# Optimization experiments

Hardware: AMD Instinct MI355X
Metric: run time of the kernel (lower is better)

## Reference

```python
import jax, jax.numpy as jnp
import numpy as np

DIM, HEADS, HDIM, B, L = 2048, 16, 128, 2, 2048

def setup_inputs() -> dict:
    key = jax.random.key(0)
    ks = jax.random.split(key, 7)
    s = 1.0 / np.sqrt(DIM)
    return {
        "x": jax.random.normal(ks[0], (B, L, DIM), jnp.float32),
        "rope_emb": jax.random.uniform(ks[1], (L, HDIM), jnp.float32),
        "wq": jax.random.normal(ks[2], (DIM, DIM), jnp.float32) * s,
        "wk": jax.random.normal(ks[3], (DIM, DIM), jnp.float32) * s,
        "wv": jax.random.normal(ks[4], (DIM, DIM), jnp.float32) * s,
        "wo": jax.random.normal(ks[5], (DIM, DIM), jnp.float32) * s,
        "bo": jnp.zeros((DIM,), jnp.float32),
    }

def _rotate_half(x):
    x1, x2 = jnp.split(x, 2, axis=-1)
    return jnp.concatenate((-x2, x1), axis=-1)

def reference(x, rope_emb, wq, wk, wv, wo, bo):
    Bq, Lq, D = x.shape
    # projections; torch Linear: y = x @ W.T, weights here stored as [out,in]
    q = jnp.einsum("bld,ed->ble", x, wq).reshape(Bq, Lq, HEADS, HDIM).transpose(0, 2, 1, 3)
    k = jnp.einsum("bld,ed->ble", x, wk).reshape(Bq, Lq, HEADS, HDIM).transpose(0, 2, 1, 3)
    v = jnp.einsum("bld,ed->ble", x, wv).reshape(Bq, Lq, HEADS, HDIM).transpose(0, 2, 1, 3)
    cos = jnp.cos(rope_emb)[None, None]  # [1,1,L,hd]
    sin = jnp.sin(rope_emb)[None, None]
    q = q * cos + _rotate_half(q) * sin
    k = k * cos + _rotate_half(k) * sin
    scale = HDIM ** -0.5
    attn = jnp.einsum("bhqd,bhkd->bhqk", q, k) * scale
    attn = jax.nn.softmax(attn, axis=-1)
    out = jnp.einsum("bhqk,bhkd->bhqd", attn, v)
    out = out.transpose(0, 2, 1, 3).reshape(Bq, Lq, D)
    return jnp.einsum("bld,ed->ble", out, wo) + bo
```

## Files before the change

kernel.cpp:

```cpp
#include <hip/hip_runtime.h>
#include <hip/hip_bf16.h>
#include <stdint.h>

#define DIMS  2048
#define HEADS 16
#define HD    128
#define BATCH 2
#define SEQ   2048
#define MROWS (BATCH*SEQ)
#define QKVN  (3*DIMS)

using bf16x8 = __attribute__((ext_vector_type(8))) short;
using f32x4  = __attribute__((ext_vector_type(4))) float;
using f32x16 = __attribute__((ext_vector_type(16))) float;
using u16x4  = __attribute__((ext_vector_type(4))) unsigned short;

__device__ __forceinline__ unsigned short f2b(float f){
    __hip_bfloat16 h = __float2bfloat16(f);
    return *reinterpret_cast<unsigned short*>(&h);
}
__device__ __forceinline__ float b2f(unsigned short u){
    __hip_bfloat16 h;
    *reinterpret_cast<unsigned short*>(&h) = u;
    return __bfloat162float(h);
}
__device__ __forceinline__ unsigned int pkbf(float lo, float hi){
    return (unsigned int)f2b(lo) | ((unsigned int)f2b(hi) << 16);
}

__device__ __forceinline__ void glds16(const void* g, void* l){
    __builtin_amdgcn_global_load_lds(
        (const __attribute__((address_space(1))) unsigned int*)g,
        (__attribute__((address_space(3))) unsigned int*)l, 16, 0, 0);
}


__global__ void k_f32bf16(const float* __restrict__ src, unsigned short* __restrict__ dst, int n4){
    int i = blockIdx.x*blockDim.x + threadIdx.x;
    if (i >= n4) return;
    const float4 v = reinterpret_cast<const float4*>(src)[i];
    u16x4 o = { f2b(v.x), f2b(v.y), f2b(v.z), f2b(v.w) };
    *reinterpret_cast<u16x4*>(dst + 4*(size_t)i) = o;
}

__global__ void k_cossin(const float* __restrict__ r, float* __restrict__ c, float* __restrict__ s, int n){
    int i = blockIdx.x*blockDim.x + threadIdx.x;
    if (i >= n) return;
    float v = r[i];
    c[i] = cosf(v);
    s[i] = sinf(v);
}

__global__ void k_rope(unsigned short* __restrict__ qkv,
                       const float* __restrict__ ct, const float* __restrict__ st){
    const int idx = blockIdx.x*blockDim.x + threadIdx.x;
    const int d0 = (idx & 7) << 3;
    const int h  = (idx >> 3) & (HEADS-1);
    const int l  = (idx >> 7) & (SEQ-1);
    const int b  = idx >> 18;

    const float4* cp = reinterpret_cast<const float4*>(ct + l*HD + d0);
    const float4* sp = reinterpret_cast<const float4*>(st + l*HD + d0);
    const float4 cl0 = cp[0],  cl1 = cp[1];
    const float4 sl0 = sp[0],  sl1 = sp[1];
    const float4 cu0 = cp[16], cu1 = cp[17];
    const float4 su0 = sp[16], su1 = sp[17];
    const float cl[8] = {cl0.x,cl0.y,cl0.z,cl0.w, cl1.x,cl1.y,cl1.z,cl1.w};
    const float sl[8] = {sl0.x,sl0.y,sl0.z,sl0.w, sl1.x,sl1.y,sl1.z,sl1.w};
    const float cu[8] = {cu0.x,cu0.y,cu0.z,cu0.w, cu1.x,cu1.y,cu1.z,cu1.w};
    const float su[8] = {su0.x,su0.y,su0.z,su0.w, su1.x,su1.y,su1.z,su1.w};

    unsigned short* base = qkv + (size_t)(b*SEQ + l)*QKVN + h*HD + d0;
    #pragma unroll
    for (int s = 0; s < 2; ++s){
        unsigned short* rp = base + s*DIMS;
        bf16x8 lo = *reinterpret_cast<const bf16x8*>(rp);
        bf16x8 hi = *reinterpret_cast<const bf16x8*>(rp + 64);
        bf16x8 olo, ohi;
        #pragma unroll
        for (int j = 0; j < 8; ++j){
            const float x1 = b2f((unsigned short)lo[j]);
            const float x2 = b2f((unsigned short)hi[j]);
            olo[j] = (short)f2b(x1*cl[j] - x2*sl[j]);
            ohi[j] = (short)f2b(x2*cu[j] + x1*su[j]);
        }
        *reinterpret_cast<bf16x8*>(rp)      = olo;
        *reinterpret_cast<bf16x8*>(rp + 64) = ohi;
    }
}

__global__ void k_vtrans(const unsigned short* __restrict__ qkv, unsigned short* __restrict__ vt){
    __shared__ unsigned short t[64*68];
    const int lt = blockIdx.x;
    const int dt = blockIdx.y;
    const int bh = blockIdx.z;
    const int b = bh >> 4, h = bh & 15;
    const int tid = threadIdx.x;
    const int l0 = lt << 6;
    #pragma unroll
    for (int it = 0; it < 4; ++it){
        const int c = tid + (it<<8);
        const int l = c >> 4;
        const int d4 = (c & 15) << 2;
        const u16x4 v = *reinterpret_cast<const u16x4*>(
            qkv + (size_t)(b*SEQ + l0 + l)*QKVN + 2*DIMS + h*HD + (dt<<6) + d4);
        *reinterpret_cast<u16x4*>(&t[l*68 + d4]) = v;
    }
    __syncthreads();
    #pragma unroll
    for (int it = 0; it < 4; ++it){
        const int c = tid + (it<<8);
        const int d = c >> 4;
        const int l4 = (c & 15) << 2;
        u16x4 o = { t[(l4+0)*68 + d], t[(l4+1)*68 + d], t[(l4+2)*68 + d], t[(l4+3)*68 + d] };
        *reinterpret_cast<u16x4*>(&vt[((size_t)bh*HD + (dt<<6) + d)*SEQ + l0 + l4]) = o;
    }
}


template<int FINAL>
__global__ __launch_bounds__(256) void k_gemm_bt(
    const unsigned short* __restrict__ A, const unsigned short* __restrict__ B,
    void* __restrict__ C, const float* __restrict__ bias, int M, int N, int K)
{
    __shared__ unsigned short lA[128*64];
    __shared__ unsigned short lB[128*64];
    const int tid  = threadIdx.x;
    const int lane = tid & 63;
    const int wave = tid >> 6;

    const int nbx = N >> 7;
    const int nwg = gridDim.x;
    const int cpx = nwg >> 3;
    const int bid = blockIdx.x;
    const int wg  = (bid & 7)*cpx + (bid >> 3);
    const int m0 = (wg / nbx) << 7;
    const int n0 = (wg % nbx) << 7;

    const int wr = (wave >> 1) << 6;
    const int wc = (wave & 1) << 6;

    f32x4 acc[4][4] = {};

    const int srow_base = (wave<<3) + (lane>>3);
    const int schunk = lane & 7;

    for (int k0 = 0; k0 < K; k0 += 64){
        #pragma unroll
        for (int i = 0; i < 4; ++i){
            const int row  = (i<<5) + srow_base;
            const int scol = k0 + ((schunk ^ (row & 7)) << 3);
            glds16(A + (size_t)(m0 + row)*K + scol, &lA[((i<<5) + (wave<<3)) << 6]);
            glds16(B + (size_t)(n0 + row)*K + scol, &lB[((i<<5) + (wave<<3)) << 6]);
        }
        __syncthreads();
        #pragma unroll
        for (int ks = 0; ks < 2; ++ks){
            bf16x8 af[4], bfr[4];
            const int colbase = (ks<<5) + ((lane>>4)<<3);
            #pragma unroll
            for (int mi = 0; mi < 4; ++mi){
                const int row = wr + (mi<<4) + (lane & 15);
                af[mi] = *reinterpret_cast<const bf16x8*>(&lA[(row<<6) + (colbase ^ ((row&7)<<3))]);
            }
            #pragma unroll
            for (int ni = 0; ni < 4; ++ni){
                const int row = wc + (ni<<4) + (lane & 15);
                bfr[ni] = *reinterpret_cast<const bf16x8*>(&lB[(row<<6) + (colbase ^ ((row&7)<<3))]);
            }
            #pragma unroll
            for (int mi = 0; mi < 4; ++mi)
                #pragma unroll
                for (int ni = 0; ni < 4; ++ni)
                    acc[mi][ni] = __builtin_amdgcn_mfma_f32_16x16x32_bf16(af[mi], bfr[ni], acc[mi][ni], 0, 0, 0);
        }
        __syncthreads();
    }

    const int r0 = (lane >> 4) << 2;
    const int cn = lane & 15;
    #pragma unroll
    for (int mi = 0; mi < 4; ++mi)
        #pragma unroll
        for (int r = 0; r < 4; ++r){
            const int gm = m0 + wr + (mi<<4) + r0 + r;
            #pragma unroll
            for (int ni = 0; ni < 4; ++ni){
                const int gn = n0 + wc + (ni<<4) + cn;
                const float v = acc[mi][ni][r];
                if (FINAL)
                    reinterpret_cast<float*>(C)[(size_t)gm*N + gn] = v + bias[gn];
                else
                    reinterpret_cast<unsigned short*>(C)[(size_t)gm*N + gn] = f2b(v);
            }
        }
}


union U8 { unsigned int w[4]; bf16x8 v; };

__global__ __launch_bounds__(512, 2) void k_attn(
    const unsigned short* __restrict__ qkv, const unsigned short* __restrict__ vt,
    unsigned short* __restrict__ aout)
{
    __shared__ unsigned short lK[2][64*128];
    __shared__ unsigned short lV[2][128*64];
    __shared__ unsigned short lO[8*32*132];

    const int tid  = threadIdx.x;
    const int lane = tid & 63;
    const int wave = tid >> 6;
    const int lq   = lane & 31;
    const int hi   = lane >> 5;
    const int bh = blockIdx.y;
    const int b = bh >> 4, h = bh & 15;
    const int q0w = (blockIdx.x << 8) + (wave << 5);

    const unsigned short* Kb = qkv + (size_t)b*SEQ*QKVN + DIMS + h*HD;
    const unsigned short* Vb = vt + (size_t)bh*HD*SEQ;

    bf16x8 qf[8];
    {
        const float qscale = 0.08838834764831845f * 1.4426950408889634f;
        const unsigned short* qp = qkv + (size_t)(b*SEQ + q0w + lq)*QKVN + h*HD + (hi<<3);
        #pragma unroll
        for (int ks = 0; ks < 8; ++ks){
            bf16x8 tv = *reinterpret_cast<const bf16x8*>(qp + (ks<<4));
            #pragma unroll
            for (int j = 0; j < 8; ++j)
                tv[j] = (short)f2b(b2f((unsigned short)tv[j]) * qscale);
            qf[ks] = tv;
        }
    }

    float m_run = -3e38f, l_run = 0.f;
    f32x16 oacc[4] = {};

    #define STAGE(pb, kv0) do { \
        _Pragma("unroll") \
        for (int i = 0; i < 2; ++i){ \
            const int kr = (wave<<3) + (i<<2) + (lane>>4); \
            glds16(Kb + (size_t)((kv0) + kr)*QKVN + (((lane&15) ^ (kr&7))<<3), \
                   &lK[pb][((wave<<3) + (i<<2))<<7]); \
            const int dr = (wave<<4) + (i<<3) + (lane>>3); \
            glds16(Vb + (size_t)dr*SEQ + (kv0) + (((lane&7) ^ (dr&7))<<3), \
                   &lV[pb][((wave<<4) + (i<<3))<<6]); \
        } \
    } while(0)

    int buf = 0;
    STAGE(0, 0);
    __syncthreads();

    for (int t = 0; t < SEQ/64; ++t){
        if (t < SEQ/64 - 1) STAGE(buf^1, (t+1)*64);

        const unsigned short* Kbuf = &lK[buf][0];
        const unsigned short* Vbuf = &lV[buf][0];

        f32x16 st0 = {}, st1 = {};
        __builtin_amdgcn_s_setprio(1);
        #pragma unroll
        for (int ks = 0; ks < 8; ++ks){
            const int col = (((ks<<1) + hi) ^ (lq & 7)) << 3;
            bf16x8 k0 = *reinterpret_cast<const bf16x8*>(&Kbuf[(lq<<7) + col]);
            bf16x8 k1 = *reinterpret_cast<const bf16x8*>(&Kbuf[((32+lq)<<7) + col]);
            st0 = __builtin_amdgcn_mfma_f32_32x32x16_bf16(k0, qf[ks], st0, 0, 0, 0);
            st1 = __builtin_amdgcn_mfma_f32_32x32x16_bf16(k1, qf[ks], st1, 0, 0, 0);
        }
        __builtin_amdgcn_s_setprio(0);

        float tmax = st0[0];
        #pragma unroll
        for (int r = 1; r < 16; ++r) tmax = fmaxf(tmax, st0[r]);
        #pragma unroll
        for (int r = 0; r < 16; ++r) tmax = fmaxf(tmax, st1[r]);
        tmax = fmaxf(tmax, __shfl_xor(tmax, 32));
        const float mnew = fmaxf(m_run, tmax);
        const float al = __builtin_amdgcn_exp2f(m_run - mnew);
        m_run = mnew;
        float tsum = 0.f;
        #pragma unroll
        for (int r = 0; r < 16; ++r){ float p = __builtin_amdgcn_exp2f(st0[r] - mnew); st0[r] = p; tsum += p; }
        #pragma unroll
        for (int r = 0; r < 16; ++r){ float p = __builtin_amdgcn_exp2f(st1[r] - mnew); st1[r] = p; tsum += p; }
        tsum += __shfl_xor(tsum, 32);
        l_run = l_run*al + tsum;
        #pragma unroll
        for (int dt = 0; dt < 4; ++dt) oacc[dt] *= al;

        bf16x8 pf[4];
        #define MAKEPF(dA, dB, SV) do { \
            unsigned int a0 = pkbf(SV[0],SV[1]),  b0 = pkbf(SV[2],SV[3]); \
            unsigned int c0 = pkbf(SV[4],SV[5]),  d0 = pkbf(SV[6],SV[7]); \
            unsigned int a1 = pkbf(SV[8],SV[9]),  b1 = pkbf(SV[10],SV[11]); \
            unsigned int c1 = pkbf(SV[12],SV[13]),d1 = pkbf(SV[14],SV[15]); \
            unsigned int ax0 = __shfl_xor(a0,32), bx0 = __shfl_xor(b0,32); \
            unsigned int cx0 = __shfl_xor(c0,32), dx0 = __shfl_xor(d0,32); \
            unsigned int ax1 = __shfl_xor(a1,32), bx1 = __shfl_xor(b1,32); \
            unsigned int cx1 = __shfl_xor(c1,32), dx1 = __shfl_xor(d1,32); \
            U8 u; \
            u.w[0] = hi ? cx0 : a0;  u.w[1] = hi ? dx0 : b0; \
            u.w[2] = hi ? c0 : ax0;  u.w[3] = hi ? d0 : bx0; \
            dA = u.v; \
            u.w[0] = hi ? cx1 : a1;  u.w[1] = hi ? dx1 : b1; \
            u.w[2] = hi ? c1 : ax1;  u.w[3] = hi ? d1 : bx1; \
            dB = u.v; \
        } while(0)
        MAKEPF(pf[0], pf[1], st0);
        MAKEPF(pf[2], pf[3], st1);
        #undef MAKEPF

        __builtin_amdgcn_s_setprio(1);
        #pragma unroll
        for (int dt = 0; dt < 4; ++dt){
            const int rowv = (dt<<5) + lq;
            #pragma unroll
            for (int f = 0; f < 4; ++f){
                const int col = (((f<<1) + hi) ^ (lq & 7)) << 3;
                bf16x8 vf = *reinterpret_cast<const bf16x8*>(&Vbuf[(rowv<<6) + col]);
                oacc[dt] = __builtin_amdgcn_mfma_f32_32x32x16_bf16(vf, pf[f], oacc[dt], 0, 0, 0);
            }
        }
        __builtin_amdgcn_s_setprio(0);

        __syncthreads();
        buf ^= 1;
    }
    #undef STAGE

    const float rl = 1.0f / l_run;
    unsigned short* oL = lO + wave*(32*132);
    #pragma unroll
    for (int dt = 0; dt < 4; ++dt)
        #pragma unroll
        for (int g = 0; g < 4; ++g){
            u16x4 w = { f2b(oacc[dt][g*4+0]*rl), f2b(oacc[dt][g*4+1]*rl),
                        f2b(oacc[dt][g*4+2]*rl), f2b(oacc[dt][g*4+3]*rl) };
            *reinterpret_cast<u16x4*>(&oL[lq*132 + (dt<<5) + (hi<<2) + (g<<3)]) = w;
        }
    #pragma unroll
    for (int i = 0; i < 16; ++i){
        const int q = (i<<1) + hi;
        u16x4 w = *reinterpret_cast<const u16x4*>(&oL[q*132 + (lq<<2)]);
        *reinterpret_cast<u16x4*>(&aout[(size_t)(b*SEQ + q0w + q)*DIMS + h*HD + (lq<<2)]) = w;
    }
}


extern "C" void kernel_launch(void* const* d_in, const int* in_sizes, int n_in,
                              void* d_out, int out_size, void* d_ws, size_t ws_size,
                              hipStream_t stream)
{
    const float* x    = (const float*)d_in[0];
    const float* rope = (const float*)d_in[1];
    const float* wq   = (const float*)d_in[2];
    const float* wk   = (const float*)d_in[3];
    const float* wv   = (const float*)d_in[4];
    const float* wo   = (const float*)d_in[5];
    const float* bo   = (const float*)d_in[6];
    float* out = (float*)d_out;

    char* ws = (char*)d_ws;
    unsigned short* x_bf   = (unsigned short*)(ws + 0);
    unsigned short* wqkv   = (unsigned short*)(ws + 16777216);
    unsigned short* wo_bf  = (unsigned short*)(ws + 41943040);
    float*          cos_t  = (float*)(ws + 50331648);
    float*          sin_t  = (float*)(ws + 51380224);
    unsigned short* qkv    = (unsigned short*)(ws + 52428800);
    unsigned short* vt     = (unsigned short*)(ws + 16777216);
    unsigned short* a_out  = (unsigned short*)(ws + 0);

    k_f32bf16<<<8192, 256, 0, stream>>>(x,  x_bf,              2097152);
    k_f32bf16<<<4096, 256, 0, stream>>>(wq, wqkv,              1048576);
    k_f32bf16<<<4096, 256, 0, stream>>>(wk, wqkv + 4194304,    1048576);
    k_f32bf16<<<4096, 256, 0, stream>>>(wv, wqkv + 8388608,    1048576);
    k_f32bf16<<<4096, 256, 0, stream>>>(wo, wo_bf,             1048576);
    k_cossin <<<1024, 256, 0, stream>>>(rope, cos_t, sin_t, SEQ*HD);

    k_gemm_bt<0><<<(MROWS/128)*(QKVN/128), 256, 0, stream>>>(x_bf, wqkv, qkv, nullptr, MROWS, QKVN, DIMS);

    k_rope<<<2048, 256, 0, stream>>>(qkv, cos_t, sin_t);

    k_vtrans<<<dim3(SEQ/64, HD/64, BATCH*HEADS), 256, 0, stream>>>(qkv, vt);

    k_attn<<<dim3(SEQ/256, BATCH*HEADS), 512, 0, stream>>>(qkv, vt, a_out);

    k_gemm_bt<1><<<(MROWS/128)*(DIMS/128), 256, 0, stream>>>(a_out, wo_bf, out, bo, MROWS, DIMS, DIMS);
}
```

Baseline: 305.7 us.

## Shrink attention blocks, defer softmax rescale, use permlane32 swap, batch weight conversion

Attention blocks drop from 512 to 256 threads covering 128 queries each. Shared memory becomes one 64 KB buffer reused for the K/V double buffers and the output staging, and each wave now stages twice as many rows. The online softmax skips the running-max update and the accumulator rescale when every lane's tile max stays within 8 (log2 units) of the current max. The cross-half P fragment exchange uses v_permlane32_swap instead of shuffles plus selects, and the four weight conversions are merged into one launch. Halving the block doubles K/V reloads per query, and the deferred max lets exponentials grow up to 2^8 before rescaling.

After: 287.5 us. 6.0% less time.

```diff
diff --git a/kernel.cpp b/kernel.cpp
--- a/kernel.cpp
+++ b/kernel.cpp
@@ -38,6 +38,19 @@
 __global__ void k_f32bf16(const float* __restrict__ src, unsigned short* __restrict__ dst, int n4){
     int i = blockIdx.x*blockDim.x + threadIdx.x;
     if (i >= n4) return;
+    const float4 v = reinterpret_cast<const float4*>(src)[i];
+    u16x4 o = { f2b(v.x), f2b(v.y), f2b(v.z), f2b(v.w) };
+    *reinterpret_cast<u16x4*>(dst + 4*(size_t)i) = o;
+}
+
+__global__ void k_wconv4(const float* __restrict__ w0, const float* __restrict__ w1,
+                         const float* __restrict__ w2, const float* __restrict__ w3,
+                         unsigned short* __restrict__ d0, unsigned short* __restrict__ d1,
+                         unsigned short* __restrict__ d2, unsigned short* __restrict__ d3){
+    const int sel = blockIdx.y;
+    const float* src = sel==0 ? w0 : sel==1 ? w1 : sel==2 ? w2 : w3;
+    unsigned short* dst = sel==0 ? d0 : sel==1 ? d1 : sel==2 ? d2 : d3;
+    const int i = blockIdx.x*blockDim.x + threadIdx.x;
     const float4 v = reinterpret_cast<const float4*>(src)[i];
     u16x4 o = { f2b(v.x), f2b(v.y), f2b(v.z), f2b(v.w) };
     *reinterpret_cast<u16x4*>(dst + 4*(size_t)i) = o;
@@ -199,13 +212,11 @@
 
 union U8 { unsigned int w[4]; bf16x8 v; };
 
-__global__ __launch_bounds__(512, 2) void k_attn(
+__global__ __launch_bounds__(256, 2) void k_attn(
     const unsigned short* __restrict__ qkv, const unsigned short* __restrict__ vt,
     unsigned short* __restrict__ aout)
 {
-    __shared__ unsigned short lK[2][64*128];
-    __shared__ unsigned short lV[2][128*64];
-    __shared__ unsigned short lO[8*32*132];
+    __shared__ unsigned short smem[32768];
 
     const int tid  = threadIdx.x;
     const int lane = tid & 63;
@@ -214,7 +225,7 @@
     const int hi   = lane >> 5;
     const int bh = blockIdx.y;
     const int b = bh >> 4, h = bh & 15;
-    const int q0w = (blockIdx.x << 8) + (wave << 5);
+    const int q0w = (blockIdx.x << 7) + (wave << 5);
 
     const unsigned short* Kb = qkv + (size_t)b*SEQ*QKVN + DIMS + h*HD;
     const unsigned short* Vb = vt + (size_t)bh*HD*SEQ;
@@ -238,13 +249,13 @@
 
     #define STAGE(pb, kv0) do { \
         _Pragma("unroll") \
-        for (int i = 0; i < 2; ++i){ \
-            const int kr = (wave<<3) + (i<<2) + (lane>>4); \
+        for (int i = 0; i < 4; ++i){ \
+            const int kr = (wave<<4) + (i<<2) + (lane>>4); \
             glds16(Kb + (size_t)((kv0) + kr)*QKVN + (((lane&15) ^ (kr&7))<<3), \
-                   &lK[pb][((wave<<3) + (i<<2))<<7]); \
-            const int dr = (wave<<4) + (i<<3) + (lane>>3); \
+                   &smem[((pb)<<13) + (((wave<<4) + (i<<2))<<7)]); \
+            const int dr = (wave<<5) + (i<<3) + (lane>>3); \
             glds16(Vb + (size_t)dr*SEQ + (kv0) + (((lane&7) ^ (dr&7))<<3), \
-                   &lV[pb][((wave<<4) + (i<<3))<<6]); \
+                   &smem[16384 + ((pb)<<13) + (((wave<<5) + (i<<3))<<6)]); \
         } \
     } while(0)
 
@@ -255,8 +266,8 @@
     for (int t = 0; t < SEQ/64; ++t){
         if (t < SEQ/64 - 1) STAGE(buf^1, (t+1)*64);
 
-        const unsigned short* Kbuf = &lK[buf][0];
-        const unsigned short* Vbuf = &lV[buf][0];
+        const unsigned short* Kbuf = &smem[buf<<13];
+        const unsigned short* Vbuf = &smem[16384 + (buf<<13)];
 
         f32x16 st0 = {}, st1 = {};
         __builtin_amdgcn_s_setprio(1);
@@ -276,18 +287,23 @@
         #pragma unroll
         for (int r = 0; r < 16; ++r) tmax = fmaxf(tmax, st1[r]);
         tmax = fmaxf(tmax, __shfl_xor(tmax, 32));
-        const float mnew = fmaxf(m_run, tmax);
-        const float al = __builtin_amdgcn_exp2f(m_run - mnew);
-        m_run = mnew;
+
+        const bool defer = __all(tmax <= m_run + 8.0f);
+        if (!defer){
+            const float mnew = fmaxf(m_run, tmax);
+            const float al = __builtin_amdgcn_exp2f(m_run - mnew);
+            m_run = mnew;
+            l_run *= al;
+            #pragma unroll
+            for (int dt = 0; dt < 4; ++dt) oacc[dt] *= al;
+        }
         float tsum = 0.f;
         #pragma unroll
-        for (int r = 0; r < 16; ++r){ float p = __builtin_amdgcn_exp2f(st0[r] - mnew); st0[r] = p; tsum += p; }
-        #pragma unroll
-        for (int r = 0; r < 16; ++r){ float p = __builtin_amdgcn_exp2f(st1[r] - mnew); st1[r] = p; tsum += p; }
+        for (int r = 0; r < 16; ++r){ float p = __builtin_amdgcn_exp2f(st0[r] - m_run); st0[r] = p; tsum += p; }
+        #pragma unroll
+        for (int r = 0; r < 16; ++r){ float p = __builtin_amdgcn_exp2f(st1[r] - m_run); st1[r] = p; tsum += p; }
         tsum += __shfl_xor(tsum, 32);
-        l_run = l_run*al + tsum;
-        #pragma unroll
-        for (int dt = 0; dt < 4; ++dt) oacc[dt] *= al;
+        l_run += tsum;
 
         bf16x8 pf[4];
         #define MAKEPF(dA, dB, SV) do { \
@@ -295,17 +311,13 @@
             unsigned int c0 = pkbf(SV[4],SV[5]),  d0 = pkbf(SV[6],SV[7]); \
             unsigned int a1 = pkbf(SV[8],SV[9]),  b1 = pkbf(SV[10],SV[11]); \
             unsigned int c1 = pkbf(SV[12],SV[13]),d1 = pkbf(SV[14],SV[15]); \
-            unsigned int ax0 = __shfl_xor(a0,32), bx0 = __shfl_xor(b0,32); \
-            unsigned int cx0 = __shfl_xor(c0,32), dx0 = __shfl_xor(d0,32); \
-            unsigned int ax1 = __shfl_xor(a1,32), bx1 = __shfl_xor(b1,32); \
-            unsigned int cx1 = __shfl_xor(c1,32), dx1 = __shfl_xor(d1,32); \
+            asm("v_permlane32_swap_b32 %0, %1" : "+v"(a0), "+v"(c0)); \
+            asm("v_permlane32_swap_b32 %0, %1" : "+v"(b0), "+v"(d0)); \
+            asm("v_permlane32_swap_b32 %0, %1" : "+v"(a1), "+v"(c1)); \
+            asm("v_permlane32_swap_b32 %0, %1" : "+v"(b1), "+v"(d1)); \
             U8 u; \
-            u.w[0] = hi ? cx0 : a0;  u.w[1] = hi ? dx0 : b0; \
-            u.w[2] = hi ? c0 : ax0;  u.w[3] = hi ? d0 : bx0; \
-            dA = u.v; \
-            u.w[0] = hi ? cx1 : a1;  u.w[1] = hi ? dx1 : b1; \
-            u.w[2] = hi ? c1 : ax1;  u.w[3] = hi ? d1 : bx1; \
-            dB = u.v; \
+            u.w[0] = a0; u.w[1] = b0; u.w[2] = c0; u.w[3] = d0; dA = u.v; \
+            u.w[0] = a1; u.w[1] = b1; u.w[2] = c1; u.w[3] = d1; dB = u.v; \
         } while(0)
         MAKEPF(pf[0], pf[1], st0);
         MAKEPF(pf[2], pf[3], st1);
@@ -330,7 +342,7 @@
     #undef STAGE
 
     const float rl = 1.0f / l_run;
-    unsigned short* oL = lO + wave*(32*132);
+    unsigned short* oL = smem + wave*(32*132);
     #pragma unroll
     for (int dt = 0; dt < 4; ++dt)
         #pragma unroll
@@ -371,11 +383,9 @@
     unsigned short* vt     = (unsigned short*)(ws + 16777216);
     unsigned short* a_out  = (unsigned short*)(ws + 0);
 
-    k_f32bf16<<<8192, 256, 0, stream>>>(x,  x_bf,              2097152);
-    k_f32bf16<<<4096, 256, 0, stream>>>(wq, wqkv,              1048576);
-    k_f32bf16<<<4096, 256, 0, stream>>>(wk, wqkv + 4194304,    1048576);
-    k_f32bf16<<<4096, 256, 0, stream>>>(wv, wqkv + 8388608,    1048576);
-    k_f32bf16<<<4096, 256, 0, stream>>>(wo, wo_bf,             1048576);
+    k_f32bf16<<<8192, 256, 0, stream>>>(x, x_bf, 2097152);
+    k_wconv4<<<dim3(4096,4), 256, 0, stream>>>(wq, wk, wv, wo,
+                                               wqkv, wqkv + 4194304, wqkv + 8388608, wo_bf);
     k_cossin <<<1024, 256, 0, stream>>>(rope, cos_t, sin_t, SEQ*HD);
 
     k_gemm_bt<0><<<(MROWS/128)*(QKVN/128), 256, 0, stream>>>(x_bf, wqkv, qkv, nullptr, MROWS, QKVN, DIMS);
@@ -384,7 +394,7 @@
 
     k_vtrans<<<dim3(SEQ/64, HD/64, BATCH*HEADS), 256, 0, stream>>>(qkv, vt);
 
-    k_attn<<<dim3(SEQ/256, BATCH*HEADS), 512, 0, stream>>>(qkv, vt, a_out);
+    k_attn<<<dim3(SEQ/128, BATCH*HEADS), 256, 0, stream>>>(qkv, vt, a_out);
 
     k_gemm_bt<1><<<(MROWS/128)*(DIMS/128), 256, 0, stream>>>(a_out, wo_bf, out, bo, MROWS, DIMS, DIMS);
 }
```
